# Kernel tuning notes

Measured on AMD Instinct MI355X. Metric: run time of the kernel, lower is better.

Reference implementation:

```python
import jax, jax.numpy as jnp
import numpy as np

N = 50000
E = 800000
IN_C = 128
OUT_C = 256
NUM_REL = 6


def _rgcn_conv(x, src, dst, etype, W, root, bias):
    # PyG RGCNConv (no bases, aggr='mean'):
    # out = x @ root + bias + sum_r mean_{j in N_r(i)}(x_j) @ W[r]
    n = x.shape[0]
    xe = x[src]  # [E, d_in] gather of source features
    out = x @ root + bias
    for r in range(NUM_REL):
        m = (etype == r)
        s = jax.ops.segment_sum(jnp.where(m[:, None], xe, 0.0), dst, num_segments=n)
        c = jax.ops.segment_sum(m.astype(x.dtype), dst, num_segments=n)
        out = out + (s / jnp.maximum(c, 1.0)[:, None]) @ W[r]
    return out


def setup_inputs() -> dict:
    key = jax.random.key(0)
    ks = jax.random.split(key, 16)
    half = OUT_C // 2

    def g(k, shape, fan_in):
        return jax.random.normal(k, shape, dtype=jnp.float32) / np.sqrt(fan_in)

    return {
        "x": jax.random.normal(ks[0], (N, IN_C), dtype=jnp.float32),
        "edge_index": jax.random.randint(ks[1], (2, E), 0, N, dtype=jnp.int32),
        "edge_type": jax.random.randint(ks[2], (E,), 0, NUM_REL, dtype=jnp.int32),
        # encoder MLP
        "enc_w0": g(ks[3], (IN_C, OUT_C), IN_C), "enc_b0": jnp.zeros((OUT_C,), jnp.float32),
        "enc_w1": g(ks[4], (OUT_C, OUT_C), OUT_C), "enc_b1": jnp.zeros((OUT_C,), jnp.float32),
        "enc_w2": g(ks[5], (OUT_C, half), OUT_C), "enc_b2": jnp.zeros((half,), jnp.float32),
        # conv1
        "W1": g(ks[6], (NUM_REL, IN_C, OUT_C), IN_C), "root1": g(ks[7], (IN_C, OUT_C), IN_C),
        "b1": jnp.zeros((OUT_C,), jnp.float32),
        # conv2
        "W2": g(ks[8], (NUM_REL, OUT_C, OUT_C), OUT_C), "root2": g(ks[9], (OUT_C, OUT_C), OUT_C),
        "b2": jnp.zeros((OUT_C,), jnp.float32),
        # conv_out
        "W3": g(ks[10], (NUM_REL, OUT_C, half), OUT_C), "root3": g(ks[11], (OUT_C, half), OUT_C),
        "b3": jnp.zeros((half,), jnp.float32),
    }


def reference(x, edge_index, edge_type,
              enc_w0, enc_b0, enc_w1, enc_b1, enc_w2, enc_b2,
              W1, root1, b1, W2, root2, b2, W3, root3, b3):
    src, dst = edge_index[0], edge_index[1]
    # dense encoder branch
    h = jax.nn.relu(x @ enc_w0 + enc_b0)
    h = jax.nn.relu(h @ enc_w1 + enc_b1)
    self_feat = h @ enc_w2 + enc_b2
    # RGCN branch
    g1 = jax.nn.relu(_rgcn_conv(x, src, dst, edge_type, W1, root1, b1))
    g2 = jax.nn.relu(_rgcn_conv(g1, src, dst, edge_type, W2, root2, b2))
    graph_feat = _rgcn_conv(g2, src, dst, edge_type, W3, root3, b3)
    return jnp.concatenate([self_feat, graph_feat], axis=-1)
```

## Files before the change

### kernel.cpp

```cpp
#include <hip/hip_runtime.h>

#define NN   50000
#define EE   800000
#define INC  128
#define OUTC 256
#define HALF 128
#define NREL 6
#define NCELL (NN * NREL)

typedef __attribute__((ext_vector_type(4))) short s16x4;
typedef __attribute__((ext_vector_type(8))) short bf16x8;
typedef __attribute__((ext_vector_type(4))) float f32x4;

__device__ __forceinline__ float b2f(short b) {
    unsigned u = ((unsigned)(unsigned short)b) << 16;
    return __uint_as_float(u);
}
__device__ __forceinline__ short f2b(float f) {
    unsigned u = __float_as_uint(f);
    unsigned r = (u + 0x7fffu + ((u >> 16) & 1u)) >> 16;
    return (short)r;
}

__device__ __forceinline__ void gload16(const void* g, void* l) {
    __builtin_amdgcn_global_load_lds(
        (const __attribute__((address_space(1))) void*)g,
        (__attribute__((address_space(3))) void*)l, 16, 0, 0);
}

__global__ __launch_bounds__(256) void count_k(const int* __restrict__ dst,
                                               const int* __restrict__ et,
                                               int* __restrict__ cnt) {
    int e = blockIdx.x * 256 + threadIdx.x;
    if (e < EE) atomicAdd(&cnt[dst[e] * NREL + et[e]], 1);
}

__global__ __launch_bounds__(256) void scanA_k(const int* __restrict__ cnt,
                                               int* __restrict__ off,
                                               int* __restrict__ bsum, int n) {
    __shared__ int sh[256];
    int t = threadIdx.x;
    int base = blockIdx.x * 512 + t * 2;
    int v0 = (base < n) ? cnt[base] : 0;
    int v1 = (base + 1 < n) ? cnt[base + 1] : 0;
    int s = v0 + v1;
    sh[t] = s; __syncthreads();
    for (int o = 1; o < 256; o <<= 1) {
        int u = (t >= o) ? sh[t - o] : 0;
        __syncthreads();
        sh[t] += u;
        __syncthreads();
    }
    int excl = sh[t] - s;
    if (base < n)     off[base]     = excl;
    if (base + 1 < n) off[base + 1] = excl + v0;
    if (t == 255) bsum[blockIdx.x] = sh[255];
}

__global__ __launch_bounds__(1024) void scanB_k(int* __restrict__ bsum, int nb) {
    __shared__ int sh[1024];
    int t = threadIdx.x;
    int s = (t < nb) ? bsum[t] : 0;
    sh[t] = s; __syncthreads();
    for (int o = 1; o < 1024; o <<= 1) {
        int u = (t >= o) ? sh[t - o] : 0;
        __syncthreads();
        sh[t] += u;
        __syncthreads();
    }
    if (t < nb) bsum[t] = sh[t] - s;
}

__global__ __launch_bounds__(256) void scanC_k(int* __restrict__ off,
                                               const int* __restrict__ bsum, int n) {
    int i = blockIdx.x * 256 + threadIdx.x;
    if (i < n) off[i] += bsum[i >> 9];
    if (i == 0) off[n] = EE;
}

__global__ __launch_bounds__(256) void copyint_k(const int* __restrict__ a,
                                                 int* __restrict__ b, int n) {
    int i = blockIdx.x * 256 + threadIdx.x;
    if (i < n) b[i] = a[i];
}

__global__ __launch_bounds__(256) void fill_k(const int* __restrict__ src,
                                              const int* __restrict__ dst,
                                              const int* __restrict__ et,
                                              int* __restrict__ cur,
                                              int* __restrict__ es) {
    int e = blockIdx.x * 256 + threadIdx.x;
    if (e < EE) {
        int key = dst[e] * NREL + et[e];
        int p = atomicAdd(&cur[key], 1);
        es[p] = src[e];
    }
}

__global__ __launch_bounds__(256) void cast_x_k(const float* __restrict__ x,
                                                short* __restrict__ xb, int n4) {
    int i = blockIdx.x * 256 + threadIdx.x;
    if (i < n4) {
        float4 v = ((const float4*)x)[i];
        s16x4 o;
        o[0] = f2b(v.x); o[1] = f2b(v.y); o[2] = f2b(v.z); o[3] = f2b(v.w);
        ((s16x4*)xb)[i] = o;
    }
}

__global__ __launch_bounds__(256) void wtcat_k(const float* __restrict__ root,
                                               const float* __restrict__ W,
                                               int K0, int Ktot, int Ncols,
                                               short* __restrict__ WT) {
    int i = blockIdx.x * 256 + threadIdx.x;
    if (i >= Ncols * Ktot) return;
    int n = i / Ktot, k = i - n * Ktot;
    float v = (k < K0) ? root[(size_t)k * Ncols + n]
                       : W[(size_t)(k - K0) * Ncols + n];
    WT[(size_t)n * Ktot + k] = f2b(v);
}

template<int D>
__global__ __launch_bounds__(256) void agg_k(const short* __restrict__ X, int ldx,
                                             const int* __restrict__ off,
                                             const int* __restrict__ es,
                                             short* __restrict__ AG, int lda,
                                             int node0, int ncells) {
    constexpr int LPC = D / 4;
    int sub  = threadIdx.x / LPC;
    int lane = threadIdx.x % LPC;
    int ci = blockIdx.x * (256 / LPC) + sub;
    if (ci >= ncells) return;
    int node = ci / NREL, rel = ci - node * NREL;
    int gcell = (node0 + node) * NREL + rel;
    int beg = off[gcell], end = off[gcell + 1];
    int c0 = lane * 4;
    float s0 = 0.f, s1 = 0.f, s2 = 0.f, s3 = 0.f;
    int j = beg;
    for (; j + 1 < end; j += 2) {
        s16x4 v = *(const s16x4*)(X + (size_t)es[j] * ldx + c0);
        s16x4 w = *(const s16x4*)(X + (size_t)es[j + 1] * ldx + c0);
        s0 += b2f(v[0]) + b2f(w[0]);
        s1 += b2f(v[1]) + b2f(w[1]);
        s2 += b2f(v[2]) + b2f(w[2]);
        s3 += b2f(v[3]) + b2f(w[3]);
    }
    if (j < end) {
        s16x4 v = *(const s16x4*)(X + (size_t)es[j] * ldx + c0);
        s0 += b2f(v[0]); s1 += b2f(v[1]); s2 += b2f(v[2]); s3 += b2f(v[3]);
    }
    float inv = (end > beg) ? 1.f / (float)(end - beg) : 0.f;
    s16x4 o;
    o[0] = f2b(s0 * inv); o[1] = f2b(s1 * inv);
    o[2] = f2b(s2 * inv); o[3] = f2b(s3 * inv);
    *(s16x4*)(AG + (size_t)node * lda + rel * D + c0) = o;
}

#define ACH(R, q) (((((R) << 2) | ((q) ^ ((R) & 3)))) * 8)

__global__ __launch_bounds__(256) void gemm_bt_k(
    const short* __restrict__ A0, int ld0,
    const short* __restrict__ A1, int ld1, int Ksplit,
    const short* __restrict__ BT,
    int M, int K, int Ncols,
    const float* __restrict__ bias, int relu,
    short* __restrict__ Cb, int ldcb,
    float* __restrict__ Cf, int ldcf) {
    __shared__ __align__(16) short As[128 * 32];
    __shared__ __align__(16) short Bs[128 * 32];
    const int tid = threadIdx.x;
    const int wave = tid >> 6, lane = tid & 63;
    const int wm = (wave & 1) * 64, wn = (wave >> 1) * 64;
    const int l16 = lane & 15, quad = lane >> 4;
    const int bm = blockIdx.x * 128, bn = blockIdx.y * 128;

    const int s0 = tid, s1 = tid + 256;
    const int r0 = s0 >> 2, c0 = (s0 & 3) ^ (r0 & 3);
    const int r1 = s1 >> 2, c1 = (s1 & 3) ^ (r1 & 3);
    short* lA0 = &As[(size_t)(wave * 64) * 8];
    short* lA1 = &As[(size_t)(256 + wave * 64) * 8];
    short* lB0 = &Bs[(size_t)(wave * 64) * 8];
    short* lB1 = &Bs[(size_t)(256 + wave * 64) * 8];

    f32x4 acc[4][4];
    #pragma unroll
    for (int i = 0; i < 4; ++i)
        #pragma unroll
        for (int j = 0; j < 4; ++j)
            acc[i][j] = (f32x4)0.f;

    for (int k0 = 0; k0 < K; k0 += 32) {
        const short* Ab; int lda; int kk;
        if (k0 < Ksplit) { Ab = A0; lda = ld0; kk = k0; }
        else             { Ab = A1; lda = ld1; kk = k0 - Ksplit; }
        gload16(Ab + (size_t)(bm + r0) * lda + kk + c0 * 8, lA0);
        gload16(Ab + (size_t)(bm + r1) * lda + kk + c1 * 8, lA1);
        gload16(BT + (size_t)(bn + r0) * K + k0 + c0 * 8, lB0);
        gload16(BT + (size_t)(bn + r1) * K + k0 + c1 * 8, lB1);
        __syncthreads();
        bf16x8 af[4], bf[4];
        #pragma unroll
        for (int mt = 0; mt < 4; ++mt)
            af[mt] = *(const bf16x8*)&As[ACH(wm + mt * 16 + l16, quad)];
        #pragma unroll
        for (int nt = 0; nt < 4; ++nt)
            bf[nt] = *(const bf16x8*)&Bs[ACH(wn + nt * 16 + l16, quad)];
        #pragma unroll
        for (int mt = 0; mt < 4; ++mt)
            #pragma unroll
            for (int nt = 0; nt < 4; ++nt)
                acc[mt][nt] = __builtin_amdgcn_mfma_f32_16x16x32_bf16(
                    af[mt], bf[nt], acc[mt][nt], 0, 0, 0);
        __syncthreads();
    }

    float bv[4];
    #pragma unroll
    for (int nt = 0; nt < 4; ++nt) bv[nt] = bias[bn + wn + nt * 16 + l16];

    #pragma unroll
    for (int mt = 0; mt < 4; ++mt) {
        int rb = bm + wm + mt * 16 + quad * 4;
        #pragma unroll
        for (int nt = 0; nt < 4; ++nt) {
            int gc = bn + wn + nt * 16 + l16;
            #pragma unroll
            for (int r = 0; r < 4; ++r) {
                int grow = rb + r;
                if (grow < M) {
                    float v = acc[mt][nt][r] + bv[nt];
                    if (relu) v = fmaxf(v, 0.f);
                    if (Cb) Cb[(size_t)grow * ldcb + gc] = f2b(v);
                    else    Cf[(size_t)grow * ldcf + gc] = v;
                }
            }
        }
    }
}

extern "C" void kernel_launch(void* const* d_in, const int* in_sizes, int n_in,
                              void* d_out, int out_size, void* d_ws, size_t ws_size,
                              hipStream_t stream) {
    const float* x      = (const float*)d_in[0];
    const int*   ei     = (const int*)d_in[1];
    const int*   srcv   = ei;
    const int*   dstv   = ei + EE;
    const int*   et     = (const int*)d_in[2];
    const float* enc_w0 = (const float*)d_in[3];
    const float* enc_b0 = (const float*)d_in[4];
    const float* enc_w1 = (const float*)d_in[5];
    const float* enc_b1 = (const float*)d_in[6];
    const float* enc_w2 = (const float*)d_in[7];
    const float* enc_b2 = (const float*)d_in[8];
    const float* W1     = (const float*)d_in[9];
    const float* root1  = (const float*)d_in[10];
    const float* b1     = (const float*)d_in[11];
    const float* W2     = (const float*)d_in[12];
    const float* root2  = (const float*)d_in[13];
    const float* b2     = (const float*)d_in[14];
    const float* W3     = (const float*)d_in[15];
    const float* root3  = (const float*)d_in[16];
    const float* b3     = (const float*)d_in[17];
    float* out = (float*)d_out;

    const int NPAD = 50048;

    char* p = (char*)d_ws;
    auto alloc = [&](size_t bytes) -> char* {
        char* r = p; p += (bytes + 255) & ~(size_t)255; return r;
    };
    short* xb  = (short*)alloc((size_t)NPAD * INC * 2);
    short* g1  = (short*)alloc((size_t)NPAD * OUTC * 2);
    short* g2  = (short*)alloc((size_t)NPAD * OUTC * 2);
    short* WT1 = (short*)alloc((size_t)OUTC * 896 * 2);
    short* WT2 = (short*)alloc((size_t)OUTC * 1792 * 2);
    short* WT3 = (short*)alloc((size_t)HALF * 1792 * 2);
    short* ET0 = (short*)alloc((size_t)OUTC * INC * 2);
    short* ET1 = (short*)alloc((size_t)OUTC * OUTC * 2);
    short* ET2 = (short*)alloc((size_t)HALF * OUTC * 2);
    int* CNT  = (int*)alloc((size_t)NCELL * 4);
    int* OFF  = (int*)alloc((size_t)(NCELL + 1) * 4);
    int* CUR  = (int*)alloc((size_t)NCELL * 4);
    int* ES   = (int*)alloc((size_t)EE * 4);
    int* BSUM = (int*)alloc(1024 * 4);
    size_t fixed = (size_t)(p - (char*)d_ws);

    int chunk = 50000;
    if (fixed + (size_t)50048 * 1536 * 2 > ws_size) chunk = 25000;
    if (chunk == 25000 && fixed + (size_t)25088 * 1536 * 2 > ws_size) chunk = 12500;
    int crpad = ((chunk + 127) / 128) * 128;
    short* AG = (short*)alloc((size_t)crpad * 1536 * 2);

    hipMemsetAsync(CNT, 0, (size_t)NCELL * 4, stream);
    count_k<<<EE / 256, 256, 0, stream>>>(dstv, et, CNT);
    int nbA = (NCELL + 511) / 512;
    scanA_k<<<nbA, 256, 0, stream>>>(CNT, OFF, BSUM, NCELL);
    scanB_k<<<1, 1024, 0, stream>>>(BSUM, nbA);
    scanC_k<<<(NCELL + 255) / 256, 256, 0, stream>>>(OFF, BSUM, NCELL);
    copyint_k<<<(NCELL + 255) / 256, 256, 0, stream>>>(OFF, CUR, NCELL);
    fill_k<<<EE / 256, 256, 0, stream>>>(srcv, dstv, et, CUR, ES);

    cast_x_k<<<(NN * INC / 4 + 255) / 256, 256, 0, stream>>>(x, xb, NN * INC / 4);
    wtcat_k<<<(OUTC * 896 + 255) / 256, 256, 0, stream>>>(root1, W1, INC, 896, OUTC, WT1);
    wtcat_k<<<(OUTC * 1792 + 255) / 256, 256, 0, stream>>>(root2, W2, OUTC, 1792, OUTC, WT2);
    wtcat_k<<<(HALF * 1792 + 255) / 256, 256, 0, stream>>>(root3, W3, OUTC, 1792, HALF, WT3);
    wtcat_k<<<(OUTC * INC + 255) / 256, 256, 0, stream>>>(enc_w0, nullptr, INC, INC, OUTC, ET0);
    wtcat_k<<<(OUTC * OUTC + 255) / 256, 256, 0, stream>>>(enc_w1, nullptr, OUTC, OUTC, OUTC, ET1);
    wtcat_k<<<(HALF * OUTC + 255) / 256, 256, 0, stream>>>(enc_w2, nullptr, OUTC, OUTC, HALF, ET2);

    auto gemm = [&](const short* A0, int ld0, const short* A1, int ld1, int Ksplit,
                    const short* BT, int M, int K, int Ncols,
                    const float* bias, int relu, short* Cb, int ldcb, float* Cf, int ldcf) {
        dim3 grid((M + 127) / 128, Ncols / 128);
        gemm_bt_k<<<grid, 256, 0, stream>>>(A0, ld0, A1, ld1, Ksplit, BT,
                                            M, K, Ncols, bias, relu, Cb, ldcb, Cf, ldcf);
    };

    gemm(xb, INC, nullptr, 0, INC, ET0, NN, INC, OUTC, enc_b0, 1, g1, OUTC, nullptr, 0);
    gemm(g1, OUTC, nullptr, 0, OUTC, ET1, NN, OUTC, OUTC, enc_b1, 1, g2, OUTC, nullptr, 0);
    gemm(g2, OUTC, nullptr, 0, OUTC, ET2, NN, OUTC, HALF, enc_b2, 0, nullptr, 0, out, OUTC);

    for (int c0 = 0; c0 < NN; c0 += chunk) {
        int nc = chunk * NREL;
        agg_k<INC><<<(nc + 7) / 8, 256, 0, stream>>>(xb, INC, OFF, ES, AG, 768, c0, nc);
        gemm(xb + (size_t)c0 * INC, INC, AG, 768, INC, WT1, chunk, 896, OUTC,
             b1, 1, g1 + (size_t)c0 * OUTC, OUTC, nullptr, 0);
    }
    for (int c0 = 0; c0 < NN; c0 += chunk) {
        int nc = chunk * NREL;
        agg_k<OUTC><<<(nc + 3) / 4, 256, 0, stream>>>(g1, OUTC, OFF, ES, AG, 1536, c0, nc);
        gemm(g1 + (size_t)c0 * OUTC, OUTC, AG, 1536, OUTC, WT2, chunk, 1792, OUTC,
             b2, 1, g2 + (size_t)c0 * OUTC, OUTC, nullptr, 0);
    }
    for (int c0 = 0; c0 < NN; c0 += chunk) {
        int nc = chunk * NREL;
        agg_k<OUTC><<<(nc + 3) / 4, 256, 0, stream>>>(g2, OUTC, OFF, ES, AG, 1536, c0, nc);
        gemm(g2 + (size_t)c0 * OUTC, OUTC, AG, 1536, OUTC, WT3, chunk, 1792, HALF,
             b3, 0, nullptr, 0, out + (size_t)c0 * OUTC + HALF, OUTC);
    }
}
```

Measured before the change: 752.5 us.

## Transform node features per relation first, then gather-mean the projected rows

Result: slower. 866.5 us (+15.1%).

```diff
diff --git a/kernel.cpp b/kernel.cpp
--- a/kernel.cpp
+++ b/kernel.cpp
@@ -7,6 +7,7 @@
 #define HALF 128
 #define NREL 6
 #define NCELL (NN * NREL)
+#define NPAD 50048
 
 typedef __attribute__((ext_vector_type(4))) short s16x4;
 typedef __attribute__((ext_vector_type(8))) short bf16x8;
@@ -108,59 +109,28 @@
     }
 }
 
-__global__ __launch_bounds__(256) void wtcat_k(const float* __restrict__ root,
-                                               const float* __restrict__ W,
-                                               int K0, int Ktot, int Ncols,
-                                               short* __restrict__ WT) {
+__global__ __launch_bounds__(256) void wtcat2_k(const float* __restrict__ root,
+                                                const float* __restrict__ W,
+                                                int K, int D, int Ncols,
+                                                short* __restrict__ BT) {
     int i = blockIdx.x * 256 + threadIdx.x;
-    if (i >= Ncols * Ktot) return;
-    int n = i / Ktot, k = i - n * Ktot;
-    float v = (k < K0) ? root[(size_t)k * Ncols + n]
-                       : W[(size_t)(k - K0) * Ncols + n];
-    WT[(size_t)n * Ktot + k] = f2b(v);
-}
-
-template<int D>
-__global__ __launch_bounds__(256) void agg_k(const short* __restrict__ X, int ldx,
-                                             const int* __restrict__ off,
-                                             const int* __restrict__ es,
-                                             short* __restrict__ AG, int lda,
-                                             int node0, int ncells) {
-    constexpr int LPC = D / 4;
-    int sub  = threadIdx.x / LPC;
-    int lane = threadIdx.x % LPC;
-    int ci = blockIdx.x * (256 / LPC) + sub;
-    if (ci >= ncells) return;
-    int node = ci / NREL, rel = ci - node * NREL;
-    int gcell = (node0 + node) * NREL + rel;
-    int beg = off[gcell], end = off[gcell + 1];
-    int c0 = lane * 4;
-    float s0 = 0.f, s1 = 0.f, s2 = 0.f, s3 = 0.f;
-    int j = beg;
-    for (; j + 1 < end; j += 2) {
-        s16x4 v = *(const s16x4*)(X + (size_t)es[j] * ldx + c0);
-        s16x4 w = *(const s16x4*)(X + (size_t)es[j + 1] * ldx + c0);
-        s0 += b2f(v[0]) + b2f(w[0]);
-        s1 += b2f(v[1]) + b2f(w[1]);
-        s2 += b2f(v[2]) + b2f(w[2]);
-        s3 += b2f(v[3]) + b2f(w[3]);
-    }
-    if (j < end) {
-        s16x4 v = *(const s16x4*)(X + (size_t)es[j] * ldx + c0);
-        s0 += b2f(v[0]); s1 += b2f(v[1]); s2 += b2f(v[2]); s3 += b2f(v[3]);
-    }
-    float inv = (end > beg) ? 1.f / (float)(end - beg) : 0.f;
-    s16x4 o;
-    o[0] = f2b(s0 * inv); o[1] = f2b(s1 * inv);
-    o[2] = f2b(s2 * inv); o[3] = f2b(s3 * inv);
-    *(s16x4*)(AG + (size_t)node * lda + rel * D + c0) = o;
-}
-
-#define ACH(R, q) (((((R) << 2) | ((q) ^ ((R) & 3)))) * 8)
+    if (i >= Ncols * K) return;
+    int n = i / K, k = i - n * K;
+    float v;
+    if (n < D) {
+        v = root[(size_t)k * D + n];
+    } else {
+        int nn = n - D;
+        int r = nn / D, c = nn - r * D;
+        v = W[((size_t)r * K + k) * D + c];
+    }
+    BT[(size_t)n * K + k] = f2b(v);
+}
+
+#define ACH(R, q) ((((R) << 2) | ((q) ^ ((R) & 3) ^ (((R) >> 2) & 1))) * 8)
 
 __global__ __launch_bounds__(256) void gemm_bt_k(
-    const short* __restrict__ A0, int ld0,
-    const short* __restrict__ A1, int ld1, int Ksplit,
+    const short* __restrict__ A, int lda,
     const short* __restrict__ BT,
     int M, int K, int Ncols,
     const float* __restrict__ bias, int relu,
@@ -175,8 +145,8 @@
     const int bm = blockIdx.x * 128, bn = blockIdx.y * 128;
 
     const int s0 = tid, s1 = tid + 256;
-    const int r0 = s0 >> 2, c0 = (s0 & 3) ^ (r0 & 3);
-    const int r1 = s1 >> 2, c1 = (s1 & 3) ^ (r1 & 3);
+    const int r0 = s0 >> 2, c0 = (s0 & 3) ^ (r0 & 3) ^ ((r0 >> 2) & 1);
+    const int r1 = s1 >> 2, c1 = (s1 & 3) ^ (r1 & 3) ^ ((r1 >> 2) & 1);
     short* lA0 = &As[(size_t)(wave * 64) * 8];
     short* lA1 = &As[(size_t)(256 + wave * 64) * 8];
     short* lB0 = &Bs[(size_t)(wave * 64) * 8];
@@ -190,11 +160,8 @@
             acc[i][j] = (f32x4)0.f;
 
     for (int k0 = 0; k0 < K; k0 += 32) {
-        const short* Ab; int lda; int kk;
-        if (k0 < Ksplit) { Ab = A0; lda = ld0; kk = k0; }
-        else             { Ab = A1; lda = ld1; kk = k0 - Ksplit; }
-        gload16(Ab + (size_t)(bm + r0) * lda + kk + c0 * 8, lA0);
-        gload16(Ab + (size_t)(bm + r1) * lda + kk + c1 * 8, lA1);
+        gload16(A + (size_t)(bm + r0) * lda + k0 + c0 * 8, lA0);
+        gload16(A + (size_t)(bm + r1) * lda + k0 + c1 * 8, lA1);
         gload16(BT + (size_t)(bn + r0) * K + k0 + c0 * 8, lB0);
         gload16(BT + (size_t)(bn + r1) * K + k0 + c1 * 8, lB1);
         __syncthreads();
@@ -216,7 +183,8 @@
 
     float bv[4];
     #pragma unroll
-    for (int nt = 0; nt < 4; ++nt) bv[nt] = bias[bn + wn + nt * 16 + l16];
+    for (int nt = 0; nt < 4; ++nt)
+        bv[nt] = bias ? bias[bn + wn + nt * 16 + l16] : 0.f;
 
     #pragma unroll
     for (int mt = 0; mt < 4; ++mt) {
@@ -235,6 +203,72 @@
                 }
             }
         }
+    }
+}
+
+template<int D>
+__global__ __launch_bounds__(256) void gagg_k(
+    const short* __restrict__ H, int ldh,
+    int rfirst, int rlast, int colbase, int self0,
+    const int* __restrict__ off, const int* __restrict__ es,
+    const float* __restrict__ accin,
+    const float* __restrict__ bias, int relu,
+    short* __restrict__ Ob, float* __restrict__ Of, int ldo) {
+    constexpr int LPN = D / 4;
+    constexpr int NPB = 256 / LPN;
+    int sub = threadIdx.x / LPN, lane = threadIdx.x % LPN;
+    int node = blockIdx.x * NPB + sub;
+    if (node >= NN) return;
+    int c0 = lane * 4;
+
+    float a0, a1, a2, a3;
+    if (accin) {
+        float4 t = *(const float4*)(accin + (size_t)node * D + c0);
+        a0 = t.x; a1 = t.y; a2 = t.z; a3 = t.w;
+    } else {
+        a0 = a1 = a2 = a3 = 0.f;
+    }
+    if (self0) {
+        s16x4 v = *(const s16x4*)(H + (size_t)node * ldh + c0);
+        a0 += b2f(v[0]); a1 += b2f(v[1]); a2 += b2f(v[2]); a3 += b2f(v[3]);
+    }
+    int cell0 = node * NREL;
+    for (int r = rfirst; r < rlast; ++r) {
+        int beg = off[cell0 + r], end = off[cell0 + r + 1];
+        if (end == beg) continue;
+        int colo = (colbase + r) * D + c0;
+        float s0 = 0.f, s1 = 0.f, s2 = 0.f, s3 = 0.f;
+        int j = beg;
+        for (; j + 1 < end; j += 2) {
+            s16x4 v = *(const s16x4*)(H + (size_t)es[j] * ldh + colo);
+            s16x4 w = *(const s16x4*)(H + (size_t)es[j + 1] * ldh + colo);
+            s0 += b2f(v[0]) + b2f(w[0]);
+            s1 += b2f(v[1]) + b2f(w[1]);
+            s2 += b2f(v[2]) + b2f(w[2]);
+            s3 += b2f(v[3]) + b2f(w[3]);
+        }
+        if (j < end) {
+            s16x4 v = *(const s16x4*)(H + (size_t)es[j] * ldh + colo);
+            s0 += b2f(v[0]); s1 += b2f(v[1]); s2 += b2f(v[2]); s3 += b2f(v[3]);
+        }
+        float inv = 1.f / (float)(end - beg);
+        a0 += s0 * inv; a1 += s1 * inv; a2 += s2 * inv; a3 += s3 * inv;
+    }
+    if (bias) {
+        float4 bv = *(const float4*)(bias + c0);
+        a0 += bv.x; a1 += bv.y; a2 += bv.z; a3 += bv.w;
+    }
+    if (relu) {
+        a0 = fmaxf(a0, 0.f); a1 = fmaxf(a1, 0.f);
+        a2 = fmaxf(a2, 0.f); a3 = fmaxf(a3, 0.f);
+    }
+    if (Ob) {
+        s16x4 o;
+        o[0] = f2b(a0); o[1] = f2b(a1); o[2] = f2b(a2); o[3] = f2b(a3);
+        *(s16x4*)(Ob + (size_t)node * ldo + c0) = o;
+    } else {
+        float4 o; o.x = a0; o.y = a1; o.z = a2; o.w = a3;
+        *(float4*)(Of + (size_t)node * ldo + c0) = o;
     }
 }
 
@@ -263,8 +297,6 @@
     const float* b3     = (const float*)d_in[17];
     float* out = (float*)d_out;
 
-    const int NPAD = 50048;
-
     char* p = (char*)d_ws;
     auto alloc = [&](size_t bytes) -> char* {
         char* r = p; p += (bytes + 255) & ~(size_t)255; return r;
@@ -272,9 +304,9 @@
     short* xb  = (short*)alloc((size_t)NPAD * INC * 2);
     short* g1  = (short*)alloc((size_t)NPAD * OUTC * 2);
     short* g2  = (short*)alloc((size_t)NPAD * OUTC * 2);
-    short* WT1 = (short*)alloc((size_t)OUTC * 896 * 2);
-    short* WT2 = (short*)alloc((size_t)OUTC * 1792 * 2);
-    short* WT3 = (short*)alloc((size_t)HALF * 1792 * 2);
+    short* BT1 = (short*)alloc((size_t)1792 * INC * 2);
+    short* BT2 = (short*)alloc((size_t)1792 * OUTC * 2);
+    short* BT3 = (short*)alloc((size_t)896 * OUTC * 2);
     short* ET0 = (short*)alloc((size_t)OUTC * INC * 2);
     short* ET1 = (short*)alloc((size_t)OUTC * OUTC * 2);
     short* ET2 = (short*)alloc((size_t)HALF * OUTC * 2);
@@ -285,11 +317,10 @@
     int* BSUM = (int*)alloc(1024 * 4);
     size_t fixed = (size_t)(p - (char*)d_ws);
 
-    int chunk = 50000;
-    if (fixed + (size_t)50048 * 1536 * 2 > ws_size) chunk = 25000;
-    if (chunk == 25000 && fixed + (size_t)25088 * 1536 * 2 > ws_size) chunk = 12500;
-    int crpad = ((chunk + 127) / 128) * 128;
-    short* AG = (short*)alloc((size_t)crpad * 1536 * 2);
+    bool fullH = fixed + (size_t)NPAD * 1792 * 2 <= ws_size;
+    short* H = (short*)alloc(fullH ? (size_t)NPAD * 1792 * 2
+                                   : (size_t)NPAD * 1024 * 2);
+    float* ACC = fullH ? nullptr : (float*)alloc((size_t)NPAD * OUTC * 4);
 
     hipMemsetAsync(CNT, 0, (size_t)NCELL * 4, stream);
     count_k<<<EE / 256, 256, 0, stream>>>(dstv, et, CNT);
@@ -301,41 +332,58 @@
     fill_k<<<EE / 256, 256, 0, stream>>>(srcv, dstv, et, CUR, ES);
 
     cast_x_k<<<(NN * INC / 4 + 255) / 256, 256, 0, stream>>>(x, xb, NN * INC / 4);
-    wtcat_k<<<(OUTC * 896 + 255) / 256, 256, 0, stream>>>(root1, W1, INC, 896, OUTC, WT1);
-    wtcat_k<<<(OUTC * 1792 + 255) / 256, 256, 0, stream>>>(root2, W2, OUTC, 1792, OUTC, WT2);
-    wtcat_k<<<(HALF * 1792 + 255) / 256, 256, 0, stream>>>(root3, W3, OUTC, 1792, HALF, WT3);
-    wtcat_k<<<(OUTC * INC + 255) / 256, 256, 0, stream>>>(enc_w0, nullptr, INC, INC, OUTC, ET0);
-    wtcat_k<<<(OUTC * OUTC + 255) / 256, 256, 0, stream>>>(enc_w1, nullptr, OUTC, OUTC, OUTC, ET1);
-    wtcat_k<<<(HALF * OUTC + 255) / 256, 256, 0, stream>>>(enc_w2, nullptr, OUTC, OUTC, HALF, ET2);
-
-    auto gemm = [&](const short* A0, int ld0, const short* A1, int ld1, int Ksplit,
-                    const short* BT, int M, int K, int Ncols,
+    auto wt = [&](const float* root, const float* W, int K, int D, int Ncols, short* BT) {
+        wtcat2_k<<<(Ncols * K + 255) / 256, 256, 0, stream>>>(root, W, K, D, Ncols, BT);
+    };
+    wt(root1, W1, INC, OUTC, 1792, BT1);
+    wt(root2, W2, OUTC, OUTC, 1792, BT2);
+    wt(root3, W3, OUTC, HALF, 896, BT3);
+    wt(enc_w0, nullptr, INC, OUTC, OUTC, ET0);
+    wt(enc_w1, nullptr, OUTC, OUTC, OUTC, ET1);
+    wt(enc_w2, nullptr, OUTC, HALF, HALF, ET2);
+
+    auto gemm = [&](const short* A, int lda, const short* BT, int M, int K, int Ncols,
                     const float* bias, int relu, short* Cb, int ldcb, float* Cf, int ldcf) {
         dim3 grid((M + 127) / 128, Ncols / 128);
-        gemm_bt_k<<<grid, 256, 0, stream>>>(A0, ld0, A1, ld1, Ksplit, BT,
-                                            M, K, Ncols, bias, relu, Cb, ldcb, Cf, ldcf);
+        gemm_bt_k<<<grid, 256, 0, stream>>>(A, lda, BT, M, K, Ncols,
+                                            bias, relu, Cb, ldcb, Cf, ldcf);
     };
 
-    gemm(xb, INC, nullptr, 0, INC, ET0, NN, INC, OUTC, enc_b0, 1, g1, OUTC, nullptr, 0);
-    gemm(g1, OUTC, nullptr, 0, OUTC, ET1, NN, OUTC, OUTC, enc_b1, 1, g2, OUTC, nullptr, 0);
-    gemm(g2, OUTC, nullptr, 0, OUTC, ET2, NN, OUTC, HALF, enc_b2, 0, nullptr, 0, out, OUTC);
-
-    for (int c0 = 0; c0 < NN; c0 += chunk) {
-        int nc = chunk * NREL;
-        agg_k<INC><<<(nc + 7) / 8, 256, 0, stream>>>(xb, INC, OFF, ES, AG, 768, c0, nc);
-        gemm(xb + (size_t)c0 * INC, INC, AG, 768, INC, WT1, chunk, 896, OUTC,
-             b1, 1, g1 + (size_t)c0 * OUTC, OUTC, nullptr, 0);
-    }
-    for (int c0 = 0; c0 < NN; c0 += chunk) {
-        int nc = chunk * NREL;
-        agg_k<OUTC><<<(nc + 3) / 4, 256, 0, stream>>>(g1, OUTC, OFF, ES, AG, 1536, c0, nc);
-        gemm(g1 + (size_t)c0 * OUTC, OUTC, AG, 1536, OUTC, WT2, chunk, 1792, OUTC,
-             b2, 1, g2 + (size_t)c0 * OUTC, OUTC, nullptr, 0);
-    }
-    for (int c0 = 0; c0 < NN; c0 += chunk) {
-        int nc = chunk * NREL;
-        agg_k<OUTC><<<(nc + 3) / 4, 256, 0, stream>>>(g2, OUTC, OFF, ES, AG, 1536, c0, nc);
-        gemm(g2 + (size_t)c0 * OUTC, OUTC, AG, 1536, OUTC, WT3, chunk, 1792, HALF,
-             b3, 0, nullptr, 0, out + (size_t)c0 * OUTC + HALF, OUTC);
-    }
-}
+    gemm(xb, INC, ET0, NN, INC, OUTC, enc_b0, 1, g1, OUTC, nullptr, 0);
+    gemm(g1, OUTC, ET1, NN, OUTC, OUTC, enc_b1, 1, g2, OUTC, nullptr, 0);
+    gemm(g2, OUTC, ET2, NN, OUTC, HALF, enc_b2, 0, nullptr, 0, out, OUTC);
+
+    auto conv = [&](const short* A, int K, int D, const short* BT,
+                    const float* bias, int relu, short* Ob, float* Of) {
+        int NPB = 256 / (D / 4);
+        int gg = (NN + NPB - 1) / NPB;
+        if (fullH) {
+            gemm(A, K, BT, NN, K, 7 * D, nullptr, 0, H, 7 * D, nullptr, 0);
+            if (D == 256)
+                gagg_k<256><<<gg, 256, 0, stream>>>(H, 7 * D, 0, NREL, 1, 1,
+                    OFF, ES, nullptr, bias, relu, Ob, Of, OUTC);
+            else
+                gagg_k<128><<<gg, 256, 0, stream>>>(H, 7 * D, 0, NREL, 1, 1,
+                    OFF, ES, nullptr, bias, relu, Ob, Of, OUTC);
+        } else {
+            gemm(A, K, BT, NN, K, 4 * D, nullptr, 0, H, 4 * D, nullptr, 0);
+            if (D == 256)
+                gagg_k<256><<<gg, 256, 0, stream>>>(H, 4 * D, 0, 3, 1, 1,
+                    OFF, ES, nullptr, nullptr, 0, nullptr, ACC, D);
+            else
+                gagg_k<128><<<gg, 256, 0, stream>>>(H, 4 * D, 0, 3, 1, 1,
+                    OFF, ES, nullptr, nullptr, 0, nullptr, ACC, D);
+            gemm(A, K, BT + (size_t)4 * D * K, NN, K, 3 * D, nullptr, 0, H, 3 * D, nullptr, 0);
+            if (D == 256)
+                gagg_k<256><<<gg, 256, 0, stream>>>(H, 3 * D, 3, NREL, -3, 0,
+                    OFF, ES, ACC, bias, relu, Ob, Of, OUTC);
+            else
+                gagg_k<128><<<gg, 256, 0, stream>>>(H, 3 * D, 3, NREL, -3, 0,
+                    OFF, ES, ACC, bias, relu, Ob, Of, OUTC);
+        }
+    };
+
+    conv(xb, INC,  OUTC, BT1, b1, 1, g1, nullptr);
+    conv(g1, OUTC, OUTC, BT2, b2, 1, g2, nullptr);
+    conv(g2, OUTC, HALF, BT3, b3, 0, nullptr, out + HALF);
+}
```

## Double-buffer GEMM LDS tiles and refine swizzle to cut bank conflicts

Applied to the files above, without the earlier changes.

Measured after the change: 773.7 us. 2.8% more time.

```diff
diff --git a/kernel.cpp b/kernel.cpp
--- a/kernel.cpp
+++ b/kernel.cpp
@@ -156,7 +156,7 @@
     *(s16x4*)(AG + (size_t)node * lda + rel * D + c0) = o;
 }
 
-#define ACH(R, q) (((((R) << 2) | ((q) ^ ((R) & 3)))) * 8)
+#define ACH(R, q) ((((R) << 2) | ((q) ^ ((R) & 3) ^ (((R) >> 2) & 1))) * 8)
 
 __global__ __launch_bounds__(256) void gemm_bt_k(
     const short* __restrict__ A0, int ld0,
@@ -166,8 +166,8 @@
     const float* __restrict__ bias, int relu,
     short* __restrict__ Cb, int ldcb,
     float* __restrict__ Cf, int ldcf) {
-    __shared__ __align__(16) short As[128 * 32];
-    __shared__ __align__(16) short Bs[128 * 32];
+    __shared__ __align__(16) short As[2][128 * 32];
+    __shared__ __align__(16) short Bs[2][128 * 32];
     const int tid = threadIdx.x;
     const int wave = tid >> 6, lane = tid & 63;
     const int wm = (wave & 1) * 64, wn = (wave >> 1) * 64;
@@ -175,12 +175,18 @@
     const int bm = blockIdx.x * 128, bn = blockIdx.y * 128;
 
     const int s0 = tid, s1 = tid + 256;
-    const int r0 = s0 >> 2, c0 = (s0 & 3) ^ (r0 & 3);
-    const int r1 = s1 >> 2, c1 = (s1 & 3) ^ (r1 & 3);
-    short* lA0 = &As[(size_t)(wave * 64) * 8];
-    short* lA1 = &As[(size_t)(256 + wave * 64) * 8];
-    short* lB0 = &Bs[(size_t)(wave * 64) * 8];
-    short* lB1 = &Bs[(size_t)(256 + wave * 64) * 8];
+    const int r0 = s0 >> 2, c0 = (s0 & 3) ^ (r0 & 3) ^ ((r0 >> 2) & 1);
+    const int r1 = s1 >> 2, c1 = (s1 & 3) ^ (r1 & 3) ^ ((r1 >> 2) & 1);
+
+    auto stage = [&](int buf, int k0) {
+        const short* Ab; int lda; int kk;
+        if (k0 < Ksplit) { Ab = A0; lda = ld0; kk = k0; }
+        else             { Ab = A1; lda = ld1; kk = k0 - Ksplit; }
+        gload16(Ab + (size_t)(bm + r0) * lda + kk + c0 * 8, &As[buf][(wave * 64) * 8]);
+        gload16(Ab + (size_t)(bm + r1) * lda + kk + c1 * 8, &As[buf][(256 + wave * 64) * 8]);
+        gload16(BT + (size_t)(bn + r0) * K + k0 + c0 * 8,   &Bs[buf][(wave * 64) * 8]);
+        gload16(BT + (size_t)(bn + r1) * K + k0 + c1 * 8,   &Bs[buf][(256 + wave * 64) * 8]);
+    };
 
     f32x4 acc[4][4];
     #pragma unroll
@@ -189,29 +195,34 @@
         for (int j = 0; j < 4; ++j)
             acc[i][j] = (f32x4)0.f;
 
-    for (int k0 = 0; k0 < K; k0 += 32) {
-        const short* Ab; int lda; int kk;
-        if (k0 < Ksplit) { Ab = A0; lda = ld0; kk = k0; }
-        else             { Ab = A1; lda = ld1; kk = k0 - Ksplit; }
-        gload16(Ab + (size_t)(bm + r0) * lda + kk + c0 * 8, lA0);
-        gload16(Ab + (size_t)(bm + r1) * lda + kk + c1 * 8, lA1);
-        gload16(BT + (size_t)(bn + r0) * K + k0 + c0 * 8, lB0);
-        gload16(BT + (size_t)(bn + r1) * K + k0 + c1 * 8, lB1);
-        __syncthreads();
+    stage(0, 0);
+    const int nk = K >> 5;
+    for (int it = 0; it < nk; ++it) {
+        const int cur = it & 1;
+        if (it + 1 < nk) {
+            stage(cur ^ 1, (it + 1) << 5);
+            asm volatile("s_waitcnt vmcnt(4)" ::: "memory");
+        } else {
+            asm volatile("s_waitcnt vmcnt(0)" ::: "memory");
+        }
+        __builtin_amdgcn_sched_barrier(0);
+        __builtin_amdgcn_s_barrier();
+        __builtin_amdgcn_sched_barrier(0);
         bf16x8 af[4], bf[4];
         #pragma unroll
         for (int mt = 0; mt < 4; ++mt)
-            af[mt] = *(const bf16x8*)&As[ACH(wm + mt * 16 + l16, quad)];
+            af[mt] = *(const bf16x8*)&As[cur][ACH(wm + mt * 16 + l16, quad)];
         #pragma unroll
         for (int nt = 0; nt < 4; ++nt)
-            bf[nt] = *(const bf16x8*)&Bs[ACH(wn + nt * 16 + l16, quad)];
+            bf[nt] = *(const bf16x8*)&Bs[cur][ACH(wn + nt * 16 + l16, quad)];
         #pragma unroll
         for (int mt = 0; mt < 4; ++mt)
             #pragma unroll
             for (int nt = 0; nt < 4; ++nt)
                 acc[mt][nt] = __builtin_amdgcn_mfma_f32_16x16x32_bf16(
                     af[mt], bf[nt], acc[mt][nt], 0, 0, 0);
-        __syncthreads();
+        __builtin_amdgcn_sched_barrier(0);
+        __builtin_amdgcn_s_barrier();
     }
 
     float bv[4];
```

## Fuse neighbor aggregation into GEMM A-tile loads and co-launch encoder GEMMs

Applied to the files above, without the earlier changes.

New measurement: 1.398 ms. 85.7% more time.

```diff
diff --git a/kernel.cpp b/kernel.cpp
--- a/kernel.cpp
+++ b/kernel.cpp
@@ -7,6 +7,7 @@
 #define HALF 128
 #define NREL 6
 #define NCELL (NN * NREL)
+#define NPAD 50048
 
 typedef __attribute__((ext_vector_type(4))) short s16x4;
 typedef __attribute__((ext_vector_type(8))) short bf16x8;
@@ -120,67 +121,43 @@
     WT[(size_t)n * Ktot + k] = f2b(v);
 }
 
-template<int D>
-__global__ __launch_bounds__(256) void agg_k(const short* __restrict__ X, int ldx,
-                                             const int* __restrict__ off,
-                                             const int* __restrict__ es,
-                                             short* __restrict__ AG, int lda,
-                                             int node0, int ncells) {
-    constexpr int LPC = D / 4;
-    int sub  = threadIdx.x / LPC;
-    int lane = threadIdx.x % LPC;
-    int ci = blockIdx.x * (256 / LPC) + sub;
-    if (ci >= ncells) return;
-    int node = ci / NREL, rel = ci - node * NREL;
-    int gcell = (node0 + node) * NREL + rel;
-    int beg = off[gcell], end = off[gcell + 1];
-    int c0 = lane * 4;
-    float s0 = 0.f, s1 = 0.f, s2 = 0.f, s3 = 0.f;
-    int j = beg;
-    for (; j + 1 < end; j += 2) {
-        s16x4 v = *(const s16x4*)(X + (size_t)es[j] * ldx + c0);
-        s16x4 w = *(const s16x4*)(X + (size_t)es[j + 1] * ldx + c0);
-        s0 += b2f(v[0]) + b2f(w[0]);
-        s1 += b2f(v[1]) + b2f(w[1]);
-        s2 += b2f(v[2]) + b2f(w[2]);
-        s3 += b2f(v[3]) + b2f(w[3]);
-    }
-    if (j < end) {
-        s16x4 v = *(const s16x4*)(X + (size_t)es[j] * ldx + c0);
-        s0 += b2f(v[0]); s1 += b2f(v[1]); s2 += b2f(v[2]); s3 += b2f(v[3]);
-    }
-    float inv = (end > beg) ? 1.f / (float)(end - beg) : 0.f;
-    s16x4 o;
-    o[0] = f2b(s0 * inv); o[1] = f2b(s1 * inv);
-    o[2] = f2b(s2 * inv); o[3] = f2b(s3 * inv);
-    *(s16x4*)(AG + (size_t)node * lda + rel * D + c0) = o;
-}
-
-#define ACH(R, q) (((((R) << 2) | ((q) ^ ((R) & 3)))) * 8)
-
-__global__ __launch_bounds__(256) void gemm_bt_k(
-    const short* __restrict__ A0, int ld0,
-    const short* __restrict__ A1, int ld1, int Ksplit,
-    const short* __restrict__ BT,
-    int M, int K, int Ncols,
-    const float* __restrict__ bias, int relu,
-    short* __restrict__ Cb, int ldcb,
-    float* __restrict__ Cf, int ldcf) {
-    __shared__ __align__(16) short As[128 * 32];
-    __shared__ __align__(16) short Bs[128 * 32];
+#define ACH(R, q) ((((R) << 2) | ((q) ^ ((R) & 3) ^ (((R) >> 2) & 1))) * 8)
+
+__global__ __launch_bounds__(256) void fgemm_k(
+    const short* __restrict__ A01, const short* __restrict__ X1,
+    const short* __restrict__ B1, int Kt1, int Ks1, int dsh1,
+    const float* __restrict__ bias1, int relu1,
+    short* __restrict__ Cb1, int ldcb1, float* __restrict__ Cf1, int ldcf1,
+    const short* __restrict__ A02, const short* __restrict__ X2,
+    const short* __restrict__ B2, int Kt2, int Ks2, int dsh2,
+    const float* __restrict__ bias2, int relu2,
+    short* __restrict__ Cb2, int ldcb2, float* __restrict__ Cf2, int ldcf2,
+    const int* __restrict__ off, const int* __restrict__ es,
+    int M, int nby1) {
+    __shared__ __align__(16) char smem[16384];
+    short* As = (short*)smem;
+    short* Bs = As + 128 * 32;
     const int tid = threadIdx.x;
     const int wave = tid >> 6, lane = tid & 63;
     const int wm = (wave & 1) * 64, wn = (wave >> 1) * 64;
     const int l16 = lane & 15, quad = lane >> 4;
-    const int bm = blockIdx.x * 128, bn = blockIdx.y * 128;
+    const int bm = blockIdx.x * 128;
+
+    const short *A0, *X, *BT; const float* bias;
+    int Kt, Ks, dsh, relu; short* Cb; int ldcb; float* Cf; int ldcf; int bn;
+    if ((int)blockIdx.y < nby1) {
+        A0 = A01; X = X1; BT = B1; Kt = Kt1; Ks = Ks1; dsh = dsh1;
+        bias = bias1; relu = relu1; Cb = Cb1; ldcb = ldcb1; Cf = Cf1; ldcf = ldcf1;
+        bn = blockIdx.y * 128;
+    } else {
+        A0 = A02; X = X2; BT = B2; Kt = Kt2; Ks = Ks2; dsh = dsh2;
+        bias = bias2; relu = relu2; Cb = Cb2; ldcb = ldcb2; Cf = Cf2; ldcf = ldcf2;
+        bn = (blockIdx.y - nby1) * 128;
+    }
 
     const int s0 = tid, s1 = tid + 256;
-    const int r0 = s0 >> 2, c0 = (s0 & 3) ^ (r0 & 3);
-    const int r1 = s1 >> 2, c1 = (s1 & 3) ^ (r1 & 3);
-    short* lA0 = &As[(size_t)(wave * 64) * 8];
-    short* lA1 = &As[(size_t)(256 + wave * 64) * 8];
-    short* lB0 = &Bs[(size_t)(wave * 64) * 8];
-    short* lB1 = &Bs[(size_t)(256 + wave * 64) * 8];
+    const int r0 = s0 >> 2, c0 = (s0 & 3) ^ (r0 & 3) ^ ((r0 >> 2) & 1);
+    const int r1 = s1 >> 2, c1 = (s1 & 3) ^ (r1 & 3) ^ ((r1 >> 2) & 1);
 
     f32x4 acc[4][4];
     #pragma unroll
@@ -189,14 +166,59 @@
         for (int j = 0; j < 4; ++j)
             acc[i][j] = (f32x4)0.f;
 
-    for (int k0 = 0; k0 < K; k0 += 32) {
-        const short* Ab; int lda; int kk;
-        if (k0 < Ksplit) { Ab = A0; lda = ld0; kk = k0; }
-        else             { Ab = A1; lda = ld1; kk = k0 - Ksplit; }
-        gload16(Ab + (size_t)(bm + r0) * lda + kk + c0 * 8, lA0);
-        gload16(Ab + (size_t)(bm + r1) * lda + kk + c1 * 8, lA1);
-        gload16(BT + (size_t)(bn + r0) * K + k0 + c0 * 8, lB0);
-        gload16(BT + (size_t)(bn + r1) * K + k0 + c1 * 8, lB1);
+    const int Dm = (1 << dsh) - 1;
+    for (int k0 = 0; k0 < Kt; k0 += 32) {
+        if (k0 < Ks) {
+            gload16(A0 + (size_t)(bm + r0) * Ks + k0 + c0 * 8, As + s0 * 8);
+            gload16(A0 + (size_t)(bm + r1) * Ks + k0 + c1 * 8, As + s1 * 8);
+        }
+        gload16(BT + (size_t)(bn + r0) * Kt + k0 + c0 * 8, Bs + s0 * 8);
+        gload16(BT + (size_t)(bn + r1) * Kt + k0 + c1 * 8, Bs + s1 * 8);
+        if (k0 >= Ks) {
+            int koff = k0 - Ks;
+            int rel = koff >> dsh, cbx = koff & Dm;
+            int q = tid & 3, rbase = tid >> 2;
+            const short* Xb = X + cbx + q * 8;
+            #pragma unroll
+            for (int pass = 0; pass < 2; ++pass) {
+                int row = pass * 64 + rbase;
+                int node = bm + row;
+                int beg = 0, end = 0;
+                if (node < NN) {
+                    int cell = node * NREL + rel;
+                    beg = off[cell]; end = off[cell + 1];
+                }
+                float a0 = 0.f, a1 = 0.f, a2 = 0.f, a3 = 0.f;
+                float a4 = 0.f, a5 = 0.f, a6 = 0.f, a7 = 0.f;
+                int j = beg;
+                for (; j + 1 < end; j += 2) {
+                    bf16x8 v = *(const bf16x8*)(Xb + ((size_t)es[j] << dsh));
+                    bf16x8 w = *(const bf16x8*)(Xb + ((size_t)es[j + 1] << dsh));
+                    a0 += b2f(v[0]) + b2f(w[0]);
+                    a1 += b2f(v[1]) + b2f(w[1]);
+                    a2 += b2f(v[2]) + b2f(w[2]);
+                    a3 += b2f(v[3]) + b2f(w[3]);
+                    a4 += b2f(v[4]) + b2f(w[4]);
+                    a5 += b2f(v[5]) + b2f(w[5]);
+                    a6 += b2f(v[6]) + b2f(w[6]);
+                    a7 += b2f(v[7]) + b2f(w[7]);
+                }
+                if (j < end) {
+                    bf16x8 v = *(const bf16x8*)(Xb + ((size_t)es[j] << dsh));
+                    a0 += b2f(v[0]); a1 += b2f(v[1]);
+                    a2 += b2f(v[2]); a3 += b2f(v[3]);
+                    a4 += b2f(v[4]); a5 += b2f(v[5]);
+                    a6 += b2f(v[6]); a7 += b2f(v[7]);
+                }
+                float inv = (end > beg) ? 1.f / (float)(end - beg) : 0.f;
+                bf16x8 o;
+                o[0] = f2b(a0 * inv); o[1] = f2b(a1 * inv);
+                o[2] = f2b(a2 * inv); o[3] = f2b(a3 * inv);
+                o[4] = f2b(a4 * inv); o[5] = f2b(a5 * inv);
+                o[6] = f2b(a6 * inv); o[7] = f2b(a7 * inv);
+                *(bf16x8*)&As[ACH(row, q)] = o;
+            }
+        }
         __syncthreads();
         bf16x8 af[4], bf[4];
         #pragma unroll
@@ -216,23 +238,61 @@
 
     float bv[4];
     #pragma unroll
-    for (int nt = 0; nt < 4; ++nt) bv[nt] = bias[bn + wn + nt * 16 + l16];
-
-    #pragma unroll
-    for (int mt = 0; mt < 4; ++mt) {
-        int rb = bm + wm + mt * 16 + quad * 4;
-        #pragma unroll
-        for (int nt = 0; nt < 4; ++nt) {
-            int gc = bn + wn + nt * 16 + l16;
-            #pragma unroll
-            for (int r = 0; r < 4; ++r) {
-                int grow = rb + r;
-                if (grow < M) {
+    for (int nt = 0; nt < 4; ++nt)
+        bv[nt] = bias ? bias[bn + wn + nt * 16 + l16] : 0.f;
+
+    if (Cb) {
+        short* Es = (short*)smem;
+        #pragma unroll
+        for (int mt = 0; mt < 4; ++mt) {
+            __syncthreads();
+            int srb = (wave & 1) * 16 + quad * 4;
+            #pragma unroll
+            for (int nt = 0; nt < 4; ++nt) {
+                int sc = wn + nt * 16 + l16;
+                #pragma unroll
+                for (int r = 0; r < 4; ++r) {
                     float v = acc[mt][nt][r] + bv[nt];
                     if (relu) v = fmaxf(v, 0.f);
-                    if (Cb) Cb[(size_t)grow * ldcb + gc] = f2b(v);
-                    else    Cf[(size_t)grow * ldcf + gc] = v;
-                }
+                    Es[(srb + r) * 128 + sc] = f2b(v);
+                }
+            }
+            __syncthreads();
+            #pragma unroll
+            for (int h = 0; h < 2; ++h) {
+                int c = tid + h * 256;
+                int rr = c >> 4, cc = c & 15;
+                int grow = bm + (rr >> 4) * 64 + mt * 16 + (rr & 15);
+                if (grow < M)
+                    *(bf16x8*)(Cb + (size_t)grow * ldcb + bn + cc * 8) =
+                        *(const bf16x8*)&Es[rr * 128 + cc * 8];
+            }
+        }
+    } else {
+        float* Ef = (float*)smem;
+        #pragma unroll
+        for (int mt = 0; mt < 4; ++mt) {
+            __syncthreads();
+            int srb = (wave & 1) * 16 + quad * 4;
+            #pragma unroll
+            for (int nt = 0; nt < 4; ++nt) {
+                int sc = wn + nt * 16 + l16;
+                #pragma unroll
+                for (int r = 0; r < 4; ++r) {
+                    float v = acc[mt][nt][r] + bv[nt];
+                    if (relu) v = fmaxf(v, 0.f);
+                    Ef[(srb + r) * 128 + sc] = v;
+                }
+            }
+            __syncthreads();
+            #pragma unroll
+            for (int h = 0; h < 4; ++h) {
+                int c = tid + h * 256;
+                int rr = c >> 5, cc = c & 31;
+                int grow = bm + (rr >> 4) * 64 + mt * 16 + (rr & 15);
+                if (grow < M)
+                    *(float4*)(Cf + (size_t)grow * ldcf + bn + cc * 4) =
+                        *(const float4*)&Ef[rr * 128 + cc * 4];
             }
         }
     }
@@ -263,8 +323,6 @@
     const float* b3     = (const float*)d_in[17];
     float* out = (float*)d_out;
 
-    const int NPAD = 50048;
-
     char* p = (char*)d_ws;
     auto alloc = [&](size_t bytes) -> char* {
         char* r = p; p += (bytes + 255) & ~(size_t)255; return r;
@@ -272,6 +330,8 @@
     short* xb  = (short*)alloc((size_t)NPAD * INC * 2);
     short* g1  = (short*)alloc((size_t)NPAD * OUTC * 2);
     short* g2  = (short*)alloc((size_t)NPAD * OUTC * 2);
+    short* e1  = (short*)alloc((size_t)NPAD * OUTC * 2);
+    short* e2  = (short*)alloc((size_t)NPAD * OUTC * 2);
     short* WT1 = (short*)alloc((size_t)OUTC * 896 * 2);
     short* WT2 = (short*)alloc((size_t)OUTC * 1792 * 2);
     short* WT3 = (short*)alloc((size_t)HALF * 1792 * 2);
@@ -283,13 +343,6 @@
     int* CUR  = (int*)alloc((size_t)NCELL * 4);
     int* ES   = (int*)alloc((size_t)EE * 4);
     int* BSUM = (int*)alloc(1024 * 4);
-    size_t fixed = (size_t)(p - (char*)d_ws);
-
-    int chunk = 50000;
-    if (fixed + (size_t)50048 * 1536 * 2 > ws_size) chunk = 25000;
-    if (chunk == 25000 && fixed + (size_t)25088 * 1536 * 2 > ws_size) chunk = 12500;
-    int crpad = ((chunk + 127) / 128) * 128;
-    short* AG = (short*)alloc((size_t)crpad * 1536 * 2);
 
     hipMemsetAsync(CNT, 0, (size_t)NCELL * 4, stream);
     count_k<<<EE / 256, 256, 0, stream>>>(dstv, et, CNT);
@@ -308,34 +361,16 @@
     wtcat_k<<<(OUTC * OUTC + 255) / 256, 256, 0, stream>>>(enc_w1, nullptr, OUTC, OUTC, OUTC, ET1);
     wtcat_k<<<(HALF * OUTC + 255) / 256, 256, 0, stream>>>(enc_w2, nullptr, OUTC, OUTC, HALF, ET2);
 
-    auto gemm = [&](const short* A0, int ld0, const short* A1, int ld1, int Ksplit,
-                    const short* BT, int M, int K, int Ncols,
-                    const float* bias, int relu, short* Cb, int ldcb, float* Cf, int ldcf) {
-        dim3 grid((M + 127) / 128, Ncols / 128);
-        gemm_bt_k<<<grid, 256, 0, stream>>>(A0, ld0, A1, ld1, Ksplit, BT,
-                                            M, K, Ncols, bias, relu, Cb, ldcb, Cf, ldcf);
-    };
-
-    gemm(xb, INC, nullptr, 0, INC, ET0, NN, INC, OUTC, enc_b0, 1, g1, OUTC, nullptr, 0);
-    gemm(g1, OUTC, nullptr, 0, OUTC, ET1, NN, OUTC, OUTC, enc_b1, 1, g2, OUTC, nullptr, 0);
-    gemm(g2, OUTC, nullptr, 0, OUTC, ET2, NN, OUTC, HALF, enc_b2, 0, nullptr, 0, out, OUTC);
-
-    for (int c0 = 0; c0 < NN; c0 += chunk) {
-        int nc = chunk * NREL;
-        agg_k<INC><<<(nc + 7) / 8, 256, 0, stream>>>(xb, INC, OFF, ES, AG, 768, c0, nc);
-        gemm(xb + (size_t)c0 * INC, INC, AG, 768, INC, WT1, chunk, 896, OUTC,
-             b1, 1, g1 + (size_t)c0 * OUTC, OUTC, nullptr, 0);
-    }
-    for (int c0 = 0; c0 < NN; c0 += chunk) {
-        int nc = chunk * NREL;
-        agg_k<OUTC><<<(nc + 3) / 4, 256, 0, stream>>>(g1, OUTC, OFF, ES, AG, 1536, c0, nc);
-        gemm(g1 + (size_t)c0 * OUTC, OUTC, AG, 1536, OUTC, WT2, chunk, 1792, OUTC,
-             b2, 1, g2 + (size_t)c0 * OUTC, OUTC, nullptr, 0);
-    }
-    for (int c0 = 0; c0 < NN; c0 += chunk) {
-        int nc = chunk * NREL;
-        agg_k<OUTC><<<(nc + 3) / 4, 256, 0, stream>>>(g2, OUTC, OFF, ES, AG, 1536, c0, nc);
-        gemm(g2 + (size_t)c0 * OUTC, OUTC, AG, 1536, OUTC, WT3, chunk, 1792, HALF,
-             b3, 0, nullptr, 0, out + (size_t)c0 * OUTC + HALF, OUTC);
-    }
-}
+    fgemm_k<<<dim3(391, 4), 256, 0, stream>>>(
+        xb, xb, WT1, 896, INC, 7, b1, 1, g1, OUTC, nullptr, 0,
+        xb, nullptr, ET0, INC, INC, 7, enc_b0, 1, e1, OUTC, nullptr, 0,
+        OFF, ES, NN, 2);
+    fgemm_k<<<dim3(391, 4), 256, 0, stream>>>(
+        g1, g1, WT2, 1792, OUTC, 8, b2, 1, g2, OUTC, nullptr, 0,
+        e1, nullptr, ET1, OUTC, OUTC, 8, enc_b1, 1, e2, OUTC, nullptr, 0,
+        OFF, ES, NN, 2);
+    fgemm_k<<<dim3(391, 2), 256, 0, stream>>>(
+        g2, g2, WT3, 1792, OUTC, 8, b3, 0, nullptr, 0, out + HALF, OUTC,
+        e2, nullptr, ET2, OUTC, OUTC, 8, enc_b2, 0, nullptr, 0, out, OUTC,
+        OFF, ES, NN, 1);
+}
```
